# Kernel tuning notes

Measured on AMD Instinct MI355X. Metric: run time of the kernel, lower is better.

The kernel has to match this reference:

```python
import jax, jax.numpy as jnp
import numpy as np

LN_EPS = 1e-5
N_NODES, N_EDGES, D_IN, D_HID, N_LAYERS = 50000, 800000, 512, 512, 3


def setup_inputs() -> dict:
    key = jax.random.key(0)
    k0, k1, k2 = jax.random.split(key, 3)
    x = jax.random.normal(k0, (N_NODES, D_IN), dtype=jnp.float32)
    edge_index = jax.random.randint(k1, (2, N_EDGES), 0, N_NODES, dtype=jnp.int32)
    # Glorot-ish scale so activations stay sane through the stack
    Ws = jax.random.normal(k2, (N_LAYERS, D_HID, D_HID), dtype=jnp.float32) / np.float32(np.sqrt(D_HID))
    bs = jnp.zeros((N_LAYERS, D_HID), dtype=jnp.float32)
    gammas = jnp.ones((N_LAYERS, D_HID), dtype=jnp.float32)
    betas = jnp.zeros((N_LAYERS, D_HID), dtype=jnp.float32)
    return {"x": x, "edge_index": edge_index, "Ws": Ws, "bs": bs, "gammas": gammas, "betas": betas}


def _layer_norm(v, gamma, beta):
    mu = jnp.mean(v, axis=-1, keepdims=True)
    vc = v - mu
    var = jnp.mean(vc * vc, axis=-1, keepdims=True)
    return gamma * vc * jax.lax.rsqrt(var + LN_EPS) + beta


def reference(x, edge_index, Ws, bs, gammas, betas):
    src, dst = edge_index[0], edge_index[1]
    n = x.shape[0]
    # GCN degrees with self-loops (graph is fixed across layers)
    deg = 1.0 + jax.ops.segment_sum(jnp.ones(src.shape[0], x.dtype), dst, num_segments=n)
    inv_sqrt = jax.lax.rsqrt(deg)
    enorm = (inv_sqrt[src] * inv_sqrt[dst])[:, None]  # [E,1] symmetric norm
    h = x
    for l in range(Ws.shape[0]):
        ht = h @ Ws[l] + bs[l]                               # [N, D] linear
        agg = jax.ops.segment_sum(ht[src] * enorm, dst, num_segments=n)
        agg = agg + ht / deg[:, None]                        # self-loop term
        # dropout is identity in eval mode; then LayerNorm -> ReLU
        h = jnp.maximum(_layer_norm(agg, gammas[l], betas[l]), 0.0)
    return h
```

## Files before the change

kernel.cpp:

```cpp
#include <hip/hip_runtime.h>

#define N_NODES 50000
#define N_EDGES 800000
#define D_FEAT 512
#define N_LAYERS 3
#define LN_EPS 1e-5f
#define M_PAD 50176
#define N_SBLK ((N_NODES + 255) / 256)
#define BUCK_STRIDE 64
#define BUCK_CAP ((size_t)N_NODES * BUCK_STRIDE + 72)

typedef __attribute__((ext_vector_type(8))) _Float16 half8;
typedef __attribute__((ext_vector_type(4))) _Float16 half4;
typedef __attribute__((ext_vector_type(4))) float f32x4;

__device__ __forceinline__ void gl_lds16(const unsigned short* g, unsigned short* l) {
  __builtin_amdgcn_global_load_lds((const __attribute__((address_space(1))) unsigned int*)g,
                                   (__attribute__((address_space(3))) unsigned int*)l, 16, 0, 0);
}


__global__ __launch_bounds__(256) void count_deg_kernel(const int* __restrict__ ei,
                                                        int* __restrict__ cnt) {
  int e = blockIdx.x * 256 + threadIdx.x;
  if (e < N_EDGES) atomicAdd(&cnt[ei[N_EDGES + e]], 1);
}

__global__ __launch_bounds__(256) void inv_sqrt_kernel(const int* __restrict__ cnt,
                                                       float* __restrict__ inv_sqrt) {
  int i = blockIdx.x * 256 + threadIdx.x;
  if (i < N_NODES) inv_sqrt[i] = rsqrtf(1.0f + (float)cnt[i]);
}

__global__ __launch_bounds__(256) void fill_bucket_kernel(const int* __restrict__ ei,
                                                          int* __restrict__ cursor,
                                                          int2* __restrict__ bucket,
                                                          const float* __restrict__ inv_sqrt) {
  int e = blockIdx.x * 256 + threadIdx.x;
  if (e < N_EDGES) {
    int s = ei[e];
    int d = ei[N_EDGES + e];
    int p = atomicAdd(&cursor[d], 1) & (BUCK_STRIDE - 1);
    int2 pk;
    pk.x = s;
    pk.y = __float_as_int(inv_sqrt[s] * inv_sqrt[d]);
    bucket[(size_t)d * BUCK_STRIDE + p] = pk;
  }
}


__global__ __launch_bounds__(256) void convert_x_kernel(const float* __restrict__ x,
                                                        _Float16* __restrict__ Ah,
                                                        _Float16* __restrict__ Al) {
  size_t i4 = ((size_t)blockIdx.x * 256 + threadIdx.x) * 4;
  int row = (int)(i4 >> 9);
  half4 h, l;
  if (row < N_NODES) {
    float4 v = *(const float4*)(x + i4);
    h[0] = (_Float16)v.x; l[0] = (_Float16)(v.x - (float)h[0]);
    h[1] = (_Float16)v.y; l[1] = (_Float16)(v.y - (float)h[1]);
    h[2] = (_Float16)v.z; l[2] = (_Float16)(v.z - (float)h[2]);
    h[3] = (_Float16)v.w; l[3] = (_Float16)(v.w - (float)h[3]);
  } else {
    h[0] = h[1] = h[2] = h[3] = (_Float16)0.f;
    l[0] = l[1] = l[2] = l[3] = (_Float16)0.f;
  }
  *(half4*)(Ah + i4) = h;
  *(half4*)(Al + i4) = l;
}

__global__ __launch_bounds__(256) void wconv_kernel(const float* __restrict__ W,
                                                    _Float16* __restrict__ Bh) {
  __shared__ float t[64][65];
  int n0 = blockIdx.x * 64, k0 = blockIdx.y * 64;
  int tid = threadIdx.x;
  int c = tid & 63, r4 = tid >> 6;
#pragma unroll
  for (int r = 0; r < 64; r += 4)
    t[r4 + r][c] = W[(size_t)(k0 + r4 + r) * D_FEAT + n0 + c];
  __syncthreads();
#pragma unroll
  for (int r = 0; r < 64; r += 4) {
    float v = t[c][r4 + r];
    Bh[(size_t)(n0 + r4 + r) * D_FEAT + k0 + c] = (_Float16)v;
  }
}


__global__ __launch_bounds__(256, 3) void mfma_gemm_kernel(
    const _Float16* __restrict__ Ah, const _Float16* __restrict__ Al,
    const _Float16* __restrict__ Bh, const float* __restrict__ bias,
    _Float16* __restrict__ ht) {
  __shared__ unsigned short sAh[128 * 32], sAl[128 * 32], sBh[128 * 32];

  int tid = threadIdx.x;
  int wave = tid >> 6, lane = tid & 63;

  int id = blockIdx.y * 4 + blockIdx.x;
  int mrow = (id & 7) + 8 * (id >> 5);
  int ncol = (id >> 3) & 3;
  int n0 = ncol * 128, m0 = mrow * 128;

  int r0 = (wave * 2 + 0) * 16 + (lane >> 2);
  int r1 = (wave * 2 + 1) * 16 + (lane >> 2);
  int s0 = (lane & 3) ^ ((r0 >> 1) & 3);
  int s1 = (lane & 3) ^ ((r1 >> 1) & 3);
  size_t gA0 = (size_t)(m0 + r0) * D_FEAT + s0 * 8;
  size_t gA1 = (size_t)(m0 + r1) * D_FEAT + s1 * 8;
  size_t gB0 = (size_t)(n0 + r0) * D_FEAT + s0 * 8;
  size_t gB1 = (size_t)(n0 + r1) * D_FEAT + s1 * 8;
  int l0 = (wave * 2 + 0) * 512;
  int l1 = (wave * 2 + 1) * 512;

  int q = lane >> 4, fr = lane & 15;
  int wm = (wave >> 1) * 64, wn = (wave & 1) * 64;
  int aoff[4], boff[4];
#pragma unroll
  for (int i = 0; i < 4; ++i) {
    int row = wm + i * 16 + fr;
    aoff[i] = row * 32 + (q ^ ((row >> 1) & 3)) * 8;
  }
#pragma unroll
  for (int j = 0; j < 4; ++j) {
    int row = wn + j * 16 + fr;
    boff[j] = row * 32 + (q ^ ((row >> 1) & 3)) * 8;
  }

  f32x4 acc[4][4];
#pragma unroll
  for (int i = 0; i < 4; ++i)
#pragma unroll
    for (int j = 0; j < 4; ++j) acc[i][j] = (f32x4)0.0f;

  for (int k0 = 0; k0 < D_FEAT; k0 += 32) {
    gl_lds16((const unsigned short*)(Ah + gA0 + k0), sAh + l0);
    gl_lds16((const unsigned short*)(Ah + gA1 + k0), sAh + l1);
    gl_lds16((const unsigned short*)(Al + gA0 + k0), sAl + l0);
    gl_lds16((const unsigned short*)(Al + gA1 + k0), sAl + l1);
    gl_lds16((const unsigned short*)(Bh + gB0 + k0), sBh + l0);
    gl_lds16((const unsigned short*)(Bh + gB1 + k0), sBh + l1);
    __syncthreads();

    half8 ah[4], al[4], bh[4];
#pragma unroll
    for (int i = 0; i < 4; ++i) ah[i] = *(const half8*)(sAh + aoff[i]);
#pragma unroll
    for (int i = 0; i < 4; ++i) al[i] = *(const half8*)(sAl + aoff[i]);
#pragma unroll
    for (int j = 0; j < 4; ++j) bh[j] = *(const half8*)(sBh + boff[j]);
#pragma unroll
    for (int i = 0; i < 4; ++i)
#pragma unroll
      for (int j = 0; j < 4; ++j)
        acc[i][j] = __builtin_amdgcn_mfma_f32_16x16x32_f16(ah[i], bh[j], acc[i][j], 0, 0, 0);
#pragma unroll
    for (int i = 0; i < 4; ++i)
#pragma unroll
      for (int j = 0; j < 4; ++j)
        acc[i][j] = __builtin_amdgcn_mfma_f32_16x16x32_f16(al[i], bh[j], acc[i][j], 0, 0, 0);
    __syncthreads();
  }

  float bj[4];
#pragma unroll
  for (int j = 0; j < 4; ++j) bj[j] = bias[n0 + wn + j * 16 + fr];
#pragma unroll
  for (int i = 0; i < 4; ++i) {
    int gm0 = m0 + wm + i * 16 + q * 4;
#pragma unroll
    for (int j = 0; j < 4; ++j) {
      int gn = n0 + wn + j * 16 + fr;
#pragma unroll
      for (int r = 0; r < 4; ++r) {
        int gm = gm0 + r;
        if (gm < N_NODES)
          ht[(size_t)gm * D_FEAT + gn] = (_Float16)(acc[i][j][r] + bj[j]);
      }
    }
  }
}


template <bool LAST>
__global__ __launch_bounds__(256) void agg_ln_relu_kernel(
    const _Float16* __restrict__ ht, const int* __restrict__ deg,
    const int2* __restrict__ bucket, const float* __restrict__ inv_sqrt,
    const float* __restrict__ gamma, const float* __restrict__ beta,
    float* __restrict__ hout, _Float16* __restrict__ ph, _Float16* __restrict__ pl) {
  int n = blockIdx.x * 4 + (threadIdx.x >> 6);
  int lane = threadIdx.x & 63;
  int c8 = lane * 8;

  half8 vself = *(const half8*)(ht + (size_t)n * D_FEAT + c8);
  float isn = inv_sqrt[n];
  int d = deg[n];

  int ng = (d + 7) >> 3;
  const int2* cp = bucket + (size_t)n * BUCK_STRIDE;

  float acc[8];
#pragma unroll
  for (int k = 0; k < 8; ++k) acc[k] = 0.f;

  if (ng > 0) {
    int2 p[8];
#pragma unroll
    for (int k = 0; k < 8; ++k) p[k] = cp[k];
    for (int g = 0; g < ng; ++g) {
      int lim = d - g * 8;
      int sx[8];
      float w[8];
#pragma unroll
      for (int k = 0; k < 8; ++k) {
        sx[k] = (k < lim) ? p[k].x : n;
        w[k] = (k < lim) ? __int_as_float(p[k].y) : 0.f;
      }
      half8 v[8];
#pragma unroll
      for (int k = 0; k < 8; ++k)
        v[k] = *(const half8*)(ht + (size_t)sx[k] * D_FEAT + c8);
#pragma unroll
      for (int k = 0; k < 8; ++k) p[k] = cp[(g + 1) * 8 + k];
#pragma unroll
      for (int k = 0; k < 8; ++k)
#pragma unroll
        for (int j = 0; j < 8; ++j) acc[j] = fmaf(w[k], (float)v[k][j], acc[j]);
    }
  }
  {
    float w = isn * isn;
#pragma unroll
    for (int k = 0; k < 8; ++k) acc[k] = fmaf(w, (float)vself[k], acc[k]);
  }

  float s = 0.f, s2 = 0.f;
#pragma unroll
  for (int k = 0; k < 8; ++k) { s += acc[k]; s2 += acc[k] * acc[k]; }
#pragma unroll
  for (int off = 32; off > 0; off >>= 1) {
    s += __shfl_xor(s, off);
    s2 += __shfl_xor(s2, off);
  }

  const float inv_d = 1.0f / (float)D_FEAT;
  float mu = s * inv_d;
  float var = s2 * inv_d - mu * mu;
  float rstd = rsqrtf(var + LN_EPS);

  float4 g0 = *(const float4*)(gamma + c8);
  float4 g1 = *(const float4*)(gamma + c8 + 4);
  float4 b0 = *(const float4*)(beta + c8);
  float4 b1 = *(const float4*)(beta + c8 + 4);
  float gg[8] = {g0.x, g0.y, g0.z, g0.w, g1.x, g1.y, g1.z, g1.w};
  float bb[8] = {b0.x, b0.y, b0.z, b0.w, b1.x, b1.y, b1.z, b1.w};

  float o[8];
#pragma unroll
  for (int k = 0; k < 8; ++k)
    o[k] = fmaxf(gg[k] * (acc[k] - mu) * rstd + bb[k], 0.f);

  if (LAST) {
    *(float4*)(hout + (size_t)n * D_FEAT + c8) = make_float4(o[0], o[1], o[2], o[3]);
    *(float4*)(hout + (size_t)n * D_FEAT + c8 + 4) = make_float4(o[4], o[5], o[6], o[7]);
  } else {
    half8 h, l;
#pragma unroll
    for (int k = 0; k < 8; ++k) {
      _Float16 hh = (_Float16)o[k];
      h[k] = hh;
      l[k] = (_Float16)(o[k] - (float)hh);
    }
    size_t off = (size_t)n * D_FEAT + c8;
    *(half8*)(ph + off) = h;
    *(half8*)(pl + off) = l;
  }
}


extern "C" void kernel_launch(void* const* d_in, const int* in_sizes, int n_in,
                              void* d_out, int out_size, void* d_ws, size_t ws_size,
                              hipStream_t stream) {
  const float* x      = (const float*)d_in[0];
  const int*   ei     = (const int*)d_in[1];
  const float* Ws     = (const float*)d_in[2];
  const float* bs     = (const float*)d_in[3];
  const float* gammas = (const float*)d_in[4];
  const float* betas  = (const float*)d_in[5];
  float* out = (float*)d_out;

  _Float16* Ah  = (_Float16*)d_ws;
  _Float16* Al  = Ah + (size_t)M_PAD * D_FEAT;
  _Float16* Bth = Al + (size_t)M_PAD * D_FEAT;
  _Float16* htb = Bth + (size_t)D_FEAT * D_FEAT;
  int2* bucket  = (int2*)(htb + (size_t)N_NODES * D_FEAT);
  float* inv_sqrt = (float*)(bucket + BUCK_CAP);
  int* deg_cnt = (int*)(inv_sqrt + N_NODES);
  int* cursor  = deg_cnt + N_NODES;

  hipMemsetAsync(deg_cnt, 0, N_NODES * sizeof(int), stream);
  hipMemsetAsync(cursor, 0, N_NODES * sizeof(int), stream);

  count_deg_kernel<<<(N_EDGES + 255) / 256, 256, 0, stream>>>(ei, deg_cnt);
  inv_sqrt_kernel<<<N_SBLK, 256, 0, stream>>>(deg_cnt, inv_sqrt);
  fill_bucket_kernel<<<(N_EDGES + 255) / 256, 256, 0, stream>>>(ei, cursor, bucket, inv_sqrt);

  convert_x_kernel<<<(M_PAD * D_FEAT / 4) / 256, 256, 0, stream>>>(x, Ah, Al);

  dim3 ggrid(D_FEAT / 128, M_PAD / 128);
  for (int l = 0; l < N_LAYERS; ++l) {
    wconv_kernel<<<dim3(8, 8), 256, 0, stream>>>(Ws + (size_t)l * D_FEAT * D_FEAT, Bth);
    mfma_gemm_kernel<<<ggrid, 256, 0, stream>>>(Ah, Al, Bth, bs + (size_t)l * D_FEAT, htb);
    if (l < N_LAYERS - 1) {
      agg_ln_relu_kernel<false><<<N_NODES / 4, 256, 0, stream>>>(
          htb, deg_cnt, bucket, inv_sqrt, gammas + (size_t)l * D_FEAT,
          betas + (size_t)l * D_FEAT, nullptr, Ah, Al);
    } else {
      agg_ln_relu_kernel<true><<<N_NODES / 4, 256, 0, stream>>>(
          htb, deg_cnt, bucket, inv_sqrt, gammas + (size_t)l * D_FEAT,
          betas + (size_t)l * D_FEAT, out, nullptr, nullptr);
    }
  }
}
```

Measured before the change: 848.7 us.

## Double-buffer GEMM LDS tiles and convert all layer weights in one launch

```diff
diff --git a/kernel.cpp b/kernel.cpp
--- a/kernel.cpp
+++ b/kernel.cpp
@@ -69,9 +69,11 @@
   *(half4*)(Al + i4) = l;
 }
 
-__global__ __launch_bounds__(256) void wconv_kernel(const float* __restrict__ W,
-                                                    _Float16* __restrict__ Bh) {
+__global__ __launch_bounds__(256) void wconv_kernel(const float* __restrict__ Ws,
+                                                    _Float16* __restrict__ Bth) {
   __shared__ float t[64][65];
+  const float* W = Ws + (size_t)blockIdx.z * D_FEAT * D_FEAT;
+  _Float16* Bh = Bth + (size_t)blockIdx.z * D_FEAT * D_FEAT;
   int n0 = blockIdx.x * 64, k0 = blockIdx.y * 64;
   int tid = threadIdx.x;
   int c = tid & 63, r4 = tid >> 6;
@@ -91,7 +93,8 @@
     const _Float16* __restrict__ Ah, const _Float16* __restrict__ Al,
     const _Float16* __restrict__ Bh, const float* __restrict__ bias,
     _Float16* __restrict__ ht) {
-  __shared__ unsigned short sAh[128 * 32], sAl[128 * 32], sBh[128 * 32];
+  __shared__ unsigned short sAh0[128 * 32], sAl0[128 * 32], sBh0[128 * 32];
+  __shared__ unsigned short sAh1[128 * 32], sAl1[128 * 32], sBh1[128 * 32];
 
   int tid = threadIdx.x;
   int wave = tid >> 6, lane = tid & 63;
@@ -132,34 +135,59 @@
 #pragma unroll
     for (int j = 0; j < 4; ++j) acc[i][j] = (f32x4)0.0f;
 
-  for (int k0 = 0; k0 < D_FEAT; k0 += 32) {
-    gl_lds16((const unsigned short*)(Ah + gA0 + k0), sAh + l0);
-    gl_lds16((const unsigned short*)(Ah + gA1 + k0), sAh + l1);
-    gl_lds16((const unsigned short*)(Al + gA0 + k0), sAl + l0);
-    gl_lds16((const unsigned short*)(Al + gA1 + k0), sAl + l1);
-    gl_lds16((const unsigned short*)(Bh + gB0 + k0), sBh + l0);
-    gl_lds16((const unsigned short*)(Bh + gB1 + k0), sBh + l1);
-    __syncthreads();
-
-    half8 ah[4], al[4], bh[4];
-#pragma unroll
-    for (int i = 0; i < 4; ++i) ah[i] = *(const half8*)(sAh + aoff[i]);
-#pragma unroll
-    for (int i = 0; i < 4; ++i) al[i] = *(const half8*)(sAl + aoff[i]);
-#pragma unroll
-    for (int j = 0; j < 4; ++j) bh[j] = *(const half8*)(sBh + boff[j]);
-#pragma unroll
-    for (int i = 0; i < 4; ++i)
-#pragma unroll
-      for (int j = 0; j < 4; ++j)
-        acc[i][j] = __builtin_amdgcn_mfma_f32_16x16x32_f16(ah[i], bh[j], acc[i][j], 0, 0, 0);
-#pragma unroll
-    for (int i = 0; i < 4; ++i)
-#pragma unroll
-      for (int j = 0; j < 4; ++j)
-        acc[i][j] = __builtin_amdgcn_mfma_f32_16x16x32_f16(al[i], bh[j], acc[i][j], 0, 0, 0);
-    __syncthreads();
-  }
+#define STAGE(S, K)                                                      \
+  do {                                                                   \
+    gl_lds16((const unsigned short*)(Ah + gA0 + (K)), sAh##S + l0);      \
+    gl_lds16((const unsigned short*)(Ah + gA1 + (K)), sAh##S + l1);      \
+    gl_lds16((const unsigned short*)(Al + gA0 + (K)), sAl##S + l0);      \
+    gl_lds16((const unsigned short*)(Al + gA1 + (K)), sAl##S + l1);      \
+    gl_lds16((const unsigned short*)(Bh + gB0 + (K)), sBh##S + l0);      \
+    gl_lds16((const unsigned short*)(Bh + gB1 + (K)), sBh##S + l1);      \
+  } while (0)
+
+#define READ(S)                                                          \
+  do {                                                                   \
+    _Pragma("unroll") for (int i = 0; i < 4; ++i) ah[i] =                \
+        *(const half8*)(sAh##S + aoff[i]);                               \
+    _Pragma("unroll") for (int i = 0; i < 4; ++i) al[i] =                \
+        *(const half8*)(sAl##S + aoff[i]);                               \
+    _Pragma("unroll") for (int j = 0; j < 4; ++j) bh[j] =                \
+        *(const half8*)(sBh##S + boff[j]);                               \
+  } while (0)
+
+#define MFMA_ALL()                                                                        \
+  do {                                                                                    \
+    _Pragma("unroll") for (int i = 0; i < 4; ++i)                                         \
+        _Pragma("unroll") for (int j = 0; j < 4; ++j) acc[i][j] =                         \
+            __builtin_amdgcn_mfma_f32_16x16x32_f16(ah[i], bh[j], acc[i][j], 0, 0, 0);     \
+    _Pragma("unroll") for (int i = 0; i < 4; ++i)                                         \
+        _Pragma("unroll") for (int j = 0; j < 4; ++j) acc[i][j] =                         \
+            __builtin_amdgcn_mfma_f32_16x16x32_f16(al[i], bh[j], acc[i][j], 0, 0, 0);     \
+  } while (0)
+
+  STAGE(0, 0);
+  __syncthreads();
+#pragma unroll
+  for (int kk = 0; kk < 8; ++kk) {
+    int k0 = kk * 64;
+    {
+      half8 ah[4], al[4], bh[4];
+      READ(0);
+      STAGE(1, k0 + 32);
+      MFMA_ALL();
+      __syncthreads();
+    }
+    {
+      half8 ah[4], al[4], bh[4];
+      READ(1);
+      if (kk < 7) STAGE(0, k0 + 64);
+      MFMA_ALL();
+      __syncthreads();
+    }
+  }
+#undef STAGE
+#undef READ
+#undef MFMA_ALL
 
   float bj[4];
 #pragma unroll
@@ -291,7 +319,7 @@
   _Float16* Ah  = (_Float16*)d_ws;
   _Float16* Al  = Ah + (size_t)M_PAD * D_FEAT;
   _Float16* Bth = Al + (size_t)M_PAD * D_FEAT;
-  _Float16* htb = Bth + (size_t)D_FEAT * D_FEAT;
+  _Float16* htb = Bth + (size_t)N_LAYERS * D_FEAT * D_FEAT;
   int2* bucket  = (int2*)(htb + (size_t)N_NODES * D_FEAT);
   float* inv_sqrt = (float*)(bucket + BUCK_CAP);
   int* deg_cnt = (int*)(inv_sqrt + N_NODES);
@@ -305,11 +333,12 @@
   fill_bucket_kernel<<<(N_EDGES + 255) / 256, 256, 0, stream>>>(ei, cursor, bucket, inv_sqrt);
 
   convert_x_kernel<<<(M_PAD * D_FEAT / 4) / 256, 256, 0, stream>>>(x, Ah, Al);
+  wconv_kernel<<<dim3(8, 8, N_LAYERS), 256, 0, stream>>>(Ws, Bth);
 
   dim3 ggrid(D_FEAT / 128, M_PAD / 128);
   for (int l = 0; l < N_LAYERS; ++l) {
-    wconv_kernel<<<dim3(8, 8), 256, 0, stream>>>(Ws + (size_t)l * D_FEAT * D_FEAT, Bth);
-    mfma_gemm_kernel<<<ggrid, 256, 0, stream>>>(Ah, Al, Bth, bs + (size_t)l * D_FEAT, htb);
+    mfma_gemm_kernel<<<ggrid, 256, 0, stream>>>(
+        Ah, Al, Bth + (size_t)l * D_FEAT * D_FEAT, bs + (size_t)l * D_FEAT, htb);
     if (l < N_LAYERS - 1) {
       agg_ln_relu_kernel<false><<<N_NODES / 4, 256, 0, stream>>>(
           htb, deg_cnt, bucket, inv_sqrt, gammas + (size_t)l * D_FEAT,
```

Result: no change. 861.7 us (+1.5%).

## Double-buffer GEMM LDS loads and batch all weight conversions into one launch

Applied to the files above, without the earlier changes.

```diff
diff --git a/kernel.cpp b/kernel.cpp
--- a/kernel.cpp
+++ b/kernel.cpp
@@ -69,9 +69,11 @@
   *(half4*)(Al + i4) = l;
 }
 
-__global__ __launch_bounds__(256) void wconv_kernel(const float* __restrict__ W,
-                                                    _Float16* __restrict__ Bh) {
+__global__ __launch_bounds__(256) void wconv_kernel(const float* __restrict__ Ws,
+                                                    _Float16* __restrict__ Bth) {
   __shared__ float t[64][65];
+  const float* W = Ws + (size_t)blockIdx.z * D_FEAT * D_FEAT;
+  _Float16* Bh = Bth + (size_t)blockIdx.z * D_FEAT * D_FEAT;
   int n0 = blockIdx.x * 64, k0 = blockIdx.y * 64;
   int tid = threadIdx.x;
   int c = tid & 63, r4 = tid >> 6;
@@ -91,7 +93,8 @@
     const _Float16* __restrict__ Ah, const _Float16* __restrict__ Al,
     const _Float16* __restrict__ Bh, const float* __restrict__ bias,
     _Float16* __restrict__ ht) {
-  __shared__ unsigned short sAh[128 * 32], sAl[128 * 32], sBh[128 * 32];
+  __shared__ unsigned short sA[2][2][128 * 32];
+  __shared__ unsigned short sB[2][128 * 32];
 
   int tid = threadIdx.x;
   int wave = tid >> 6, lane = tid & 63;
@@ -132,22 +135,39 @@
 #pragma unroll
     for (int j = 0; j < 4; ++j) acc[i][j] = (f32x4)0.0f;
 
-  for (int k0 = 0; k0 < D_FEAT; k0 += 32) {
-    gl_lds16((const unsigned short*)(Ah + gA0 + k0), sAh + l0);
-    gl_lds16((const unsigned short*)(Ah + gA1 + k0), sAh + l1);
-    gl_lds16((const unsigned short*)(Al + gA0 + k0), sAl + l0);
-    gl_lds16((const unsigned short*)(Al + gA1 + k0), sAl + l1);
-    gl_lds16((const unsigned short*)(Bh + gB0 + k0), sBh + l0);
-    gl_lds16((const unsigned short*)(Bh + gB1 + k0), sBh + l1);
-    __syncthreads();
+  auto stage = [&](int b, int K) {
+    gl_lds16((const unsigned short*)(Ah + gA0 + K), &sA[b][0][l0]);
+    gl_lds16((const unsigned short*)(Ah + gA1 + K), &sA[b][0][l1]);
+    gl_lds16((const unsigned short*)(Al + gA0 + K), &sA[b][1][l0]);
+    gl_lds16((const unsigned short*)(Al + gA1 + K), &sA[b][1][l1]);
+    gl_lds16((const unsigned short*)(Bh + gB0 + K), &sB[b][l0]);
+    gl_lds16((const unsigned short*)(Bh + gB1 + K), &sB[b][l1]);
+  };
+
+  stage(0, 0);
+#pragma unroll
+  for (int kk = 0; kk < 16; ++kk) {
+    const int cur = kk & 1;
+    __builtin_amdgcn_sched_barrier(0);
+    __builtin_amdgcn_s_barrier();
+    if (kk < 15) {
+      stage(cur ^ 1, (kk + 1) * 32);
+      asm volatile("s_waitcnt vmcnt(6)" ::: "memory");
+    } else {
+      asm volatile("s_waitcnt vmcnt(0)" ::: "memory");
+    }
+    __builtin_amdgcn_sched_barrier(0);
+    __builtin_amdgcn_s_barrier();
+    __builtin_amdgcn_sched_barrier(0);
 
     half8 ah[4], al[4], bh[4];
 #pragma unroll
-    for (int i = 0; i < 4; ++i) ah[i] = *(const half8*)(sAh + aoff[i]);
-#pragma unroll
-    for (int i = 0; i < 4; ++i) al[i] = *(const half8*)(sAl + aoff[i]);
-#pragma unroll
-    for (int j = 0; j < 4; ++j) bh[j] = *(const half8*)(sBh + boff[j]);
+    for (int i = 0; i < 4; ++i) ah[i] = *(const half8*)(&sA[cur][0][aoff[i]]);
+#pragma unroll
+    for (int i = 0; i < 4; ++i) al[i] = *(const half8*)(&sA[cur][1][aoff[i]]);
+#pragma unroll
+    for (int j = 0; j < 4; ++j) bh[j] = *(const half8*)(&sB[cur][boff[j]]);
+    __builtin_amdgcn_s_setprio(1);
 #pragma unroll
     for (int i = 0; i < 4; ++i)
 #pragma unroll
@@ -158,7 +178,7 @@
 #pragma unroll
       for (int j = 0; j < 4; ++j)
         acc[i][j] = __builtin_amdgcn_mfma_f32_16x16x32_f16(al[i], bh[j], acc[i][j], 0, 0, 0);
-    __syncthreads();
+    __builtin_amdgcn_s_setprio(0);
   }
 
   float bj[4];
@@ -291,7 +311,7 @@
   _Float16* Ah  = (_Float16*)d_ws;
   _Float16* Al  = Ah + (size_t)M_PAD * D_FEAT;
   _Float16* Bth = Al + (size_t)M_PAD * D_FEAT;
-  _Float16* htb = Bth + (size_t)D_FEAT * D_FEAT;
+  _Float16* htb = Bth + (size_t)N_LAYERS * D_FEAT * D_FEAT;
   int2* bucket  = (int2*)(htb + (size_t)N_NODES * D_FEAT);
   float* inv_sqrt = (float*)(bucket + BUCK_CAP);
   int* deg_cnt = (int*)(inv_sqrt + N_NODES);
@@ -305,11 +325,12 @@
   fill_bucket_kernel<<<(N_EDGES + 255) / 256, 256, 0, stream>>>(ei, cursor, bucket, inv_sqrt);
 
   convert_x_kernel<<<(M_PAD * D_FEAT / 4) / 256, 256, 0, stream>>>(x, Ah, Al);
+  wconv_kernel<<<dim3(8, 8, N_LAYERS), 256, 0, stream>>>(Ws, Bth);
 
   dim3 ggrid(D_FEAT / 128, M_PAD / 128);
   for (int l = 0; l < N_LAYERS; ++l) {
-    wconv_kernel<<<dim3(8, 8), 256, 0, stream>>>(Ws + (size_t)l * D_FEAT * D_FEAT, Bth);
-    mfma_gemm_kernel<<<ggrid, 256, 0, stream>>>(Ah, Al, Bth, bs + (size_t)l * D_FEAT, htb);
+    mfma_gemm_kernel<<<ggrid, 256, 0, stream>>>(
+        Ah, Al, Bth + (size_t)l * D_FEAT * D_FEAT, bs + (size_t)l * D_FEAT, htb);
     if (l < N_LAYERS - 1) {
       agg_ln_relu_kernel<false><<<N_NODES / 4, 256, 0, stream>>>(
           htb, deg_cnt, bucket, inv_sqrt, gammas + (size_t)l * D_FEAT,
```

Result: no change. 856.2 us (+0.9%).

## Fuse x fp32-to-fp16 split into first GEMM and batch weight conversion

Applied to the files above, without the earlier changes.

```diff
diff --git a/kernel.cpp b/kernel.cpp
--- a/kernel.cpp
+++ b/kernel.cpp
@@ -48,30 +48,11 @@
   }
 }
 
-
-__global__ __launch_bounds__(256) void convert_x_kernel(const float* __restrict__ x,
-                                                        _Float16* __restrict__ Ah,
-                                                        _Float16* __restrict__ Al) {
-  size_t i4 = ((size_t)blockIdx.x * 256 + threadIdx.x) * 4;
-  int row = (int)(i4 >> 9);
-  half4 h, l;
-  if (row < N_NODES) {
-    float4 v = *(const float4*)(x + i4);
-    h[0] = (_Float16)v.x; l[0] = (_Float16)(v.x - (float)h[0]);
-    h[1] = (_Float16)v.y; l[1] = (_Float16)(v.y - (float)h[1]);
-    h[2] = (_Float16)v.z; l[2] = (_Float16)(v.z - (float)h[2]);
-    h[3] = (_Float16)v.w; l[3] = (_Float16)(v.w - (float)h[3]);
-  } else {
-    h[0] = h[1] = h[2] = h[3] = (_Float16)0.f;
-    l[0] = l[1] = l[2] = l[3] = (_Float16)0.f;
-  }
-  *(half4*)(Ah + i4) = h;
-  *(half4*)(Al + i4) = l;
-}
-
-__global__ __launch_bounds__(256) void wconv_kernel(const float* __restrict__ W,
-                                                    _Float16* __restrict__ Bh) {
+__global__ __launch_bounds__(256) void wconv_kernel(const float* __restrict__ Ws,
+                                                    _Float16* __restrict__ Bth) {
   __shared__ float t[64][65];
+  const float* W = Ws + (size_t)blockIdx.z * D_FEAT * D_FEAT;
+  _Float16* Bh = Bth + (size_t)blockIdx.z * D_FEAT * D_FEAT;
   int n0 = blockIdx.x * 64, k0 = blockIdx.y * 64;
   int tid = threadIdx.x;
   int c = tid & 63, r4 = tid >> 6;
@@ -87,10 +68,11 @@
 }
 
 
+template <bool FP32A>
 __global__ __launch_bounds__(256, 3) void mfma_gemm_kernel(
     const _Float16* __restrict__ Ah, const _Float16* __restrict__ Al,
-    const _Float16* __restrict__ Bh, const float* __restrict__ bias,
-    _Float16* __restrict__ ht) {
+    const float* __restrict__ Xf, const _Float16* __restrict__ Bh,
+    const float* __restrict__ bias, _Float16* __restrict__ ht) {
   __shared__ unsigned short sAh[128 * 32], sAl[128 * 32], sBh[128 * 32];
 
   int tid = threadIdx.x;
@@ -112,6 +94,14 @@
   int l0 = (wave * 2 + 0) * 512;
   int l1 = (wave * 2 + 1) * 512;
 
+  size_t gX0 = 0, gX1 = 0;
+  if (FP32A) {
+    int rr0 = (m0 + r0 < N_NODES) ? (m0 + r0) : (N_NODES - 1);
+    int rr1 = (m0 + r1 < N_NODES) ? (m0 + r1) : (N_NODES - 1);
+    gX0 = (size_t)rr0 * D_FEAT + s0 * 8;
+    gX1 = (size_t)rr1 * D_FEAT + s1 * 8;
+  }
+
   int q = lane >> 4, fr = lane & 15;
   int wm = (wave >> 1) * 64, wn = (wave & 1) * 64;
   int aoff[4], boff[4];
@@ -133,10 +123,29 @@
     for (int j = 0; j < 4; ++j) acc[i][j] = (f32x4)0.0f;
 
   for (int k0 = 0; k0 < D_FEAT; k0 += 32) {
-    gl_lds16((const unsigned short*)(Ah + gA0 + k0), sAh + l0);
-    gl_lds16((const unsigned short*)(Ah + gA1 + k0), sAh + l1);
-    gl_lds16((const unsigned short*)(Al + gA0 + k0), sAl + l0);
-    gl_lds16((const unsigned short*)(Al + gA1 + k0), sAl + l1);
+    if constexpr (FP32A) {
+      const float* p0 = Xf + gX0 + k0;
+      const float* p1 = Xf + gX1 + k0;
+      float4 a0 = *(const float4*)p0, b0 = *(const float4*)(p0 + 4);
+      float4 a1 = *(const float4*)p1, b1 = *(const float4*)(p1 + 4);
+      float f0[8] = {a0.x, a0.y, a0.z, a0.w, b0.x, b0.y, b0.z, b0.w};
+      float f1[8] = {a1.x, a1.y, a1.z, a1.w, b1.x, b1.y, b1.z, b1.w};
+      half8 h0, lo0, h1, lo1;
+#pragma unroll
+      for (int k = 0; k < 8; ++k) {
+        _Float16 t0 = (_Float16)f0[k]; h0[k] = t0; lo0[k] = (_Float16)(f0[k] - (float)t0);
+        _Float16 t1 = (_Float16)f1[k]; h1[k] = t1; lo1[k] = (_Float16)(f1[k] - (float)t1);
+      }
+      *(half8*)(sAh + l0 + lane * 8) = h0;
+      *(half8*)(sAl + l0 + lane * 8) = lo0;
+      *(half8*)(sAh + l1 + lane * 8) = h1;
+      *(half8*)(sAl + l1 + lane * 8) = lo1;
+    } else {
+      gl_lds16((const unsigned short*)(Ah + gA0 + k0), sAh + l0);
+      gl_lds16((const unsigned short*)(Ah + gA1 + k0), sAh + l1);
+      gl_lds16((const unsigned short*)(Al + gA0 + k0), sAl + l0);
+      gl_lds16((const unsigned short*)(Al + gA1 + k0), sAl + l1);
+    }
     gl_lds16((const unsigned short*)(Bh + gB0 + k0), sBh + l0);
     gl_lds16((const unsigned short*)(Bh + gB1 + k0), sBh + l1);
     __syncthreads();
@@ -291,7 +300,7 @@
   _Float16* Ah  = (_Float16*)d_ws;
   _Float16* Al  = Ah + (size_t)M_PAD * D_FEAT;
   _Float16* Bth = Al + (size_t)M_PAD * D_FEAT;
-  _Float16* htb = Bth + (size_t)D_FEAT * D_FEAT;
+  _Float16* htb = Bth + (size_t)N_LAYERS * D_FEAT * D_FEAT;
   int2* bucket  = (int2*)(htb + (size_t)N_NODES * D_FEAT);
   float* inv_sqrt = (float*)(bucket + BUCK_CAP);
   int* deg_cnt = (int*)(inv_sqrt + N_NODES);
@@ -299,17 +308,26 @@
 
   hipMemsetAsync(deg_cnt, 0, N_NODES * sizeof(int), stream);
   hipMemsetAsync(cursor, 0, N_NODES * sizeof(int), stream);
+  hipMemsetAsync(Ah + (size_t)N_NODES * D_FEAT, 0,
+                 (size_t)(M_PAD - N_NODES) * D_FEAT * sizeof(_Float16), stream);
+  hipMemsetAsync(Al + (size_t)N_NODES * D_FEAT, 0,
+                 (size_t)(M_PAD - N_NODES) * D_FEAT * sizeof(_Float16), stream);
 
   count_deg_kernel<<<(N_EDGES + 255) / 256, 256, 0, stream>>>(ei, deg_cnt);
   inv_sqrt_kernel<<<N_SBLK, 256, 0, stream>>>(deg_cnt, inv_sqrt);
   fill_bucket_kernel<<<(N_EDGES + 255) / 256, 256, 0, stream>>>(ei, cursor, bucket, inv_sqrt);
 
-  convert_x_kernel<<<(M_PAD * D_FEAT / 4) / 256, 256, 0, stream>>>(x, Ah, Al);
+  wconv_kernel<<<dim3(8, 8, N_LAYERS), 256, 0, stream>>>(Ws, Bth);
 
   dim3 ggrid(D_FEAT / 128, M_PAD / 128);
   for (int l = 0; l < N_LAYERS; ++l) {
-    wconv_kernel<<<dim3(8, 8), 256, 0, stream>>>(Ws + (size_t)l * D_FEAT * D_FEAT, Bth);
-    mfma_gemm_kernel<<<ggrid, 256, 0, stream>>>(Ah, Al, Bth, bs + (size_t)l * D_FEAT, htb);
+    if (l == 0) {
+      mfma_gemm_kernel<true><<<ggrid, 256, 0, stream>>>(
+          Ah, Al, x, Bth, bs, htb);
+    } else {
+      mfma_gemm_kernel<false><<<ggrid, 256, 0, stream>>>(
+          Ah, Al, x, Bth + (size_t)l * D_FEAT * D_FEAT, bs + (size_t)l * D_FEAT, htb);
+    }
     if (l < N_LAYERS - 1) {
       agg_ln_relu_kernel<false><<<N_NODES / 4, 256, 0, stream>>>(
           htb, deg_cnt, bucket, inv_sqrt, gammas + (size_t)l * D_FEAT,
```

New measurement: 813.8 us. -4.1%, faster.
